# Optimization experiments

Measured on AMD Instinct MI355X. Metric: run time of the kernel, lower is better.

The kernel has to match this reference:

```python
import jax, jax.numpy as jnp
import numpy as np
from jax import lax

B, C, H, W = 16, 64, 56, 56


def _conv2d(x, w, b, dilation, padding):
    y = lax.conv_general_dilated(
        x, w, window_strides=(1, 1),
        padding=((padding, padding), (padding, padding)),
        rhs_dilation=(dilation, dilation),
        dimension_numbers=('NCHW', 'OIHW', 'NCHW'))
    return y + b[None, :, None, None]


def setup_inputs() -> dict:
    key = jax.random.key(0)
    k1, k2, k3 = jax.random.split(key, 3)
    x = jax.random.normal(k1, (B, C, H, W), dtype=jnp.float32)
    w1 = jax.random.normal(k2, (128, C, 7, 7), dtype=jnp.float32) * 0.05
    b1 = jnp.zeros((128,), dtype=jnp.float32)
    w2 = jax.random.normal(k3, (49, 128, 1, 1), dtype=jnp.float32) * 0.05
    b2 = jnp.zeros((49,), dtype=jnp.float32)
    return {"x": x, "w1": w1, "b1": b1, "w2": w2, "b2": b2}


def reference(x, w1, b1, w2, b2):
    b_, c_, h_, w_ = x.shape
    # attention-kernel branch: conv(7x7, dil=2) -> 1x1 -> softmax over 49 channels
    k = _conv2d(x, w1, b1, dilation=2, padding=6)
    k = _conv2d(k, w2, b2, dilation=1, padding=0)
    attn = jax.nn.softmax(k, axis=1)  # [B, 49, H, W]

    # dilated 13x13 neighborhood sampled at stride-2 offsets -> 7x7 taps per pixel
    xp = jnp.pad(x, ((0, 0), (0, 0), (6, 6), (6, 6)))
    shifts = [xp[:, :, 2 * p:2 * p + h_, 2 * q:2 * q + w_]
              for p in range(7) for q in range(7)]
    patches = jnp.stack(shifts, axis=-1)  # [B, C, H, W, 49]

    # Faithful to torch .view/.reshape semantics (row-major): the original code
    # reshapes [B,C,H,W,kk] -> groups of size C and [B,49,H,W] -> [B*H*W,7,7]
    # WITHOUT permuting, so the group<->pixel correspondence is the row-major one.
    pg = patches.reshape(b_ * h_ * w_, c_, 49)  # == torch view(1,-1,C,13,13)[::2,::2]
    kg = attn.reshape(b_ * h_ * w_, 49)         # == torch reshape(B*H*W,1,1,7,7)
    out = jnp.einsum('gck,gk->gc', pg, kg)      # grouped conv3d, groups=B*H*W
    return out.reshape(b_, c_, h_, w_)
```

## Files before the change

### kernel.cpp

```cpp
#include <hip/hip_runtime.h>
#include <hip/hip_bf16.h>

#define HW 3136
#define NPIX 50176

typedef __attribute__((ext_vector_type(8))) _Float16 f16x8;
typedef __attribute__((ext_vector_type(4))) float f32x4;
typedef __attribute__((ext_vector_type(8))) unsigned short u16x8;

__device__ inline unsigned short f2h(float v){
    _Float16 h = (_Float16)v;
    union { _Float16 h; unsigned short u; } cv; cv.h = h; return cv.u;
}
__device__ inline float h2f(unsigned short u){
    union { unsigned short u; _Float16 h; } cv; cv.u = u; return (float)cv.h;
}

__global__ __launch_bounds__(256) void prep_all(
    const float* __restrict__ x, const float* __restrict__ w1,
    unsigned short* __restrict__ xg, unsigned short* __restrict__ w1t,
    unsigned short* __restrict__ xpad)
{
    int bb = blockIdx.x;
    if (bb < 392) {
        int t = bb * 256 + threadIdx.x;
        int g = t / NPIX;
        int pix = t - g * NPIX;
        int b = pix / HW; int s = pix - b * HW;
        const float* xp = x + (size_t)b * 64 * HW + (size_t)g * 32 * HW + s;
        unsigned short* dst = xg + ((size_t)(b * 2 + g) * HW + s) * 32;
#pragma unroll
        for (int p = 0; p < 4; ++p) {
            alignas(16) unsigned short tmp[8];
#pragma unroll
            for (int e = 0; e < 8; ++e)
                tmp[e] = f2h(xp[(size_t)(p * 8 + e) * HW]);
            *(u16x8*)(dst + p * 8) = *(const u16x8*)tmp;
        }
    } else if (bb < 664) {
        int t2 = (bb - 392) * 256 + threadIdx.x;
        int plane = t2 / 68; int r = t2 - plane * 68;
        unsigned short* dst = xpad + ((size_t)plane * 68 + r) * 72;
        int h = r - 6;
        alignas(16) unsigned short tmp[72];
#pragma unroll
        for (int i = 0; i < 72; ++i) tmp[i] = 0;
        if (h >= 0 && h < 56) {
            const float* src = x + (size_t)plane * HW + h * 56;
#pragma unroll
            for (int wq = 0; wq < 56; ++wq) tmp[6 + wq] = f2h(src[wq]);
        }
#pragma unroll
        for (int k = 0; k < 9; ++k)
            *(u16x8*)(dst + k * 8) = *(const u16x8*)(tmp + k * 8);
    } else {
        int t = (bb - 664) * 256 + threadIdx.x;
        if (t < 2 * 49 * 128) {
            int g = t / (49 * 128);
            int r = t - g * 49 * 128;
            int tap = r / 128; int oc = r - tap * 128;
            unsigned short* dst = w1t + (size_t)t * 32;
            for (int ic = 0; ic < 32; ++ic)
                dst[ic] = f2h(w1[((size_t)oc * 64 + g * 32 + ic) * 49 + tap]);
        }
    }
}

#define LOADA(Abuf, tap) do {                                                 \
    const int p_ = (tap) / 7, q_ = (tap) - 7 * ((tap) / 7);                   \
    const int off_ = p_ * 9792 + q_ * 144;                                    \
    _Pragma("unroll")                                                         \
    for (int mt = 0; mt < 7; ++mt)                                            \
        Abuf[mt] = *(const f16x8*)(smem + abase[mt] + off_);                  \
    } while (0)

#define LOADB(Bbuf, tap) do {                                                 \
    const unsigned short* p_ = wb + (size_t)(tap) * 4096;                     \
    Bbuf[0] = *(const f16x8*)(p_);                                            \
    Bbuf[1] = *(const f16x8*)(p_ + 512);                                      \
    Bbuf[2] = *(const f16x8*)(p_ + 1024);                                     \
    Bbuf[3] = *(const f16x8*)(p_ + 1536);                                     \
    } while (0)

#define DOMFMA(Abuf, Bbuf) do {                                               \
    __builtin_amdgcn_s_setprio(1);                                            \
    _Pragma("unroll")                                                         \
    for (int mt = 0; mt < 7; ++mt) {                                          \
        acc[mt][0] = __builtin_amdgcn_mfma_f32_16x16x32_f16(Abuf[mt], Bbuf[0], acc[mt][0], 0, 0, 0); \
        acc[mt][1] = __builtin_amdgcn_mfma_f32_16x16x32_f16(Abuf[mt], Bbuf[1], acc[mt][1], 0, 0, 0); \
        acc[mt][2] = __builtin_amdgcn_mfma_f32_16x16x32_f16(Abuf[mt], Bbuf[2], acc[mt][2], 0, 0, 0); \
        acc[mt][3] = __builtin_amdgcn_mfma_f32_16x16x32_f16(Abuf[mt], Bbuf[3], acc[mt][3], 0, 0, 0); \
    }                                                                         \
    __builtin_amdgcn_s_setprio(0);                                            \
    } while (0)

__global__ __launch_bounds__(512, 2) void conv_full(
    const unsigned short* __restrict__ xg, const unsigned short* __restrict__ w1t,
    const float* __restrict__ b1, const float* __restrict__ w2,
    const float* __restrict__ b2, unsigned short* __restrict__ attn)
{
    __shared__ char smem[156672];
    unsigned short* k1sa = (unsigned short*)smem;
    unsigned short* w2s  = (unsigned short*)(smem + 60928);
    unsigned short* k1sb = (unsigned short*)(smem + 78336);

    const int blk = blockIdx.x;
    const int b   = blk / 14; const int rg = blk - b * 14;
    const int h0  = rg * 4;
    const int tid = threadIdx.x;
    const int lane = tid & 63, warp = tid >> 6;
    const int g   = warp >> 2;
    const int wm  = (warp >> 1) & 1, wn = warp & 1;
    const int oc0 = wn * 64;
    const int li  = lane & 15, j = lane >> 4;

    const unsigned short* xplane[2] = {
        xg + (size_t)(b * 2 + 0) * HW * 32,
        xg + (size_t)(b * 2 + 1) * HW * 32 };

    u16x8 zz; for (int e = 0; e < 8; ++e) zz[e] = 0;

    u16x8 sv[14];
#pragma unroll
    for (int u = 0; u < 14; ++u) {
        int i = u * 512 + tid;
        int pl = i / 3584; int rem = i - pl * 3584;
        int row = rem / 224; int r2 = rem - row * 224;
        int site = r2 >> 2, chunk = r2 & 3;
        int hh = h0 - 6 + row;
        sv[u] = (hh >= 0 && hh < 56)
            ? *(const u16x8*)(xplane[pl] + ((size_t)hh * 56 + site) * 32 + chunk * 8)
            : zz;
    }

    {
        f32x4 zv = {0.f, 0.f, 0.f, 0.f};
#pragma unroll
        for (int u = 0; u < 20; ++u) {
            int i = u * 512 + tid;
            if (i < 9792) *(f32x4*)(smem + (size_t)i * 16) = zv;
        }
    }
    __syncthreads();

#pragma unroll
    for (int u = 0; u < 14; ++u) {
        int i = u * 512 + tid;
        int pl = i / 3584; int rem = i - pl * 3584;
        int row = rem / 224; int r2 = rem - row * 224;
        int site = r2 >> 2, chunk = r2 & 3;
        int hh = h0 - 6 + row;
        if (hh >= 0 && hh < 56)
            *(u16x8*)(smem + pl * 78336 + (row * 68 + 6 + site) * 72 + chunk * 16) = sv[u];
    }
    __syncthreads();

    int abase[7];
#pragma unroll
    for (int mt = 0; mt < 7; ++mt) {
        int local = wm * 112 + mt * 16 + li;
        int rb = local / 56; int wp = local - rb * 56;
        abase[mt] = g * 78336 + (rb * 68 + wp) * 72 + j * 16;
    }

    f32x4 acc[7][4];
#pragma unroll
    for (int mt = 0; mt < 7; ++mt)
#pragma unroll
        for (int nt = 0; nt < 4; ++nt)
#pragma unroll
            for (int c = 0; c < 4; ++c) acc[mt][nt][c] = 0.f;

    const unsigned short* wb = w1t + ((size_t)g * 49 * 128 + oc0 + li) * 32 + j * 8;

    {
        f16x8 A[2][7], B[3][4];
        LOADA(A[0], 0); LOADB(B[0], 0); LOADB(B[1], 1);
#pragma unroll
        for (int t = 0; t < 49; ++t) {
            if (t < 48) LOADA(A[(t + 1) & 1], t + 1);
            if (t < 47) LOADB(B[(t + 2) % 3], t + 2);
            __builtin_amdgcn_sched_barrier(0x8);
            DOMFMA(A[t & 1], B[t % 3]);
            __builtin_amdgcn_sched_barrier(0x8);
        }
    }

    f32x4 wv[4];
#pragma unroll
    for (int u = 0; u < 4; ++u) {
        int idx = u * 512 + tid;
        wv[u] = (idx < 1568) ? *(const f32x4*)(w2 + (size_t)idx * 4)
                             : (f32x4){0.f, 0.f, 0.f, 0.f};
    }

    __syncthreads();

    {
        unsigned short* kb = g ? k1sb : k1sa;
        const int pixbase = wm * 112;
#pragma unroll
        for (int nt = 0; nt < 4; ++nt) {
            int oc = oc0 + nt * 16 + li;
            float bias = g ? 0.f : b1[oc];
#pragma unroll
            for (int mt = 0; mt < 7; ++mt) {
#pragma unroll
                for (int i = 0; i < 4; ++i) {
                    int px = pixbase + mt * 16 + j * 4 + i;
                    kb[px * 136 + oc] = f2h(acc[mt][nt][i] + bias);
                }
            }
        }
    }
#pragma unroll
    for (int u = 0; u < 4; ++u) {
        int idx = u * 512 + tid;
        if (idx < 1568) {
            int a = idx / 32; int c0 = (idx - a * 32) * 4;
            alignas(8) unsigned short t4[4];
#pragma unroll
            for (int e = 0; e < 4; ++e) t4[e] = f2h(wv[u][e]);
            *(unsigned long long*)(w2s + a * 136 + c0) = *(const unsigned long long*)t4;
        }
    }
    __syncthreads();

    const int start = (warp < 6) ? warp * 2 : 12 + (warp - 6);
    const int cnt   = (warp < 6) ? 2 : 1;
    unsigned short* ab = attn + (size_t)b * 49 * HW;

#pragma unroll
    for (int u = 0; u < 2; ++u) {
        if (u < cnt) {
            int pxt = start + u;
            f32x4 a2[4];
#pragma unroll
            for (int tt = 0; tt < 4; ++tt)
#pragma unroll
                for (int c = 0; c < 4; ++c) a2[tt][c] = 0.f;
#pragma unroll
            for (int ks = 0; ks < 4; ++ks) {
                const f16x8 ba = *(const f16x8*)(k1sa + (pxt * 16 + li) * 136 + ks * 32 + j * 8);
                const f16x8 bbv = *(const f16x8*)(k1sb + (pxt * 16 + li) * 136 + ks * 32 + j * 8);
                const f16x8 bf = ba + bbv;
#pragma unroll
                for (int tt = 0; tt < 4; ++tt) {
                    const f16x8 af = *(const f16x8*)(w2s + (tt * 16 + li) * 136 + ks * 32 + j * 8);
                    a2[tt] = __builtin_amdgcn_mfma_f32_16x16x32_f16(af, bf, a2[tt], 0, 0, 0);
                }
            }
            float mx = -3e38f;
#pragma unroll
            for (int tt = 0; tt < 4; ++tt)
#pragma unroll
                for (int i = 0; i < 4; ++i) {
                    int r = tt * 16 + j * 4 + i;
                    float v = a2[tt][i] + ((r < 49) ? b2[r] : 0.f);
                    a2[tt][i] = v;
                    if (r < 49) mx = fmaxf(mx, v);
                }
            mx = fmaxf(mx, __shfl_xor(mx, 16));
            mx = fmaxf(mx, __shfl_xor(mx, 32));
            float sum = 0.f; float ex[16];
#pragma unroll
            for (int tt = 0; tt < 4; ++tt)
#pragma unroll
                for (int i = 0; i < 4; ++i) {
                    int r = tt * 16 + j * 4 + i;
                    float e = (r < 49) ? __expf(a2[tt][i] - mx) : 0.f;
                    ex[tt * 4 + i] = e; sum += e;
                }
            sum += __shfl_xor(sum, 16);
            sum += __shfl_xor(sum, 32);
            float inv = 1.f / sum;

            int s = rg * 224 + pxt * 16 + li;
#pragma unroll
            for (int tt = 0; tt < 4; ++tt)
#pragma unroll
                for (int i = 0; i < 4; ++i) {
                    int r = tt * 16 + j * 4 + i;
                    if (r < 49) ab[(size_t)r * HW + s] = f2h(ex[tt * 4 + i] * inv);
                }
        }
    }
}

__global__ __launch_bounds__(256) void gather_kernel(
    const unsigned short* __restrict__ xpad, const unsigned short* __restrict__ attn,
    float* __restrict__ out)
{
    int tid = blockIdx.x * 256 + threadIdx.x;
    int plane = tid / 392;
    int r1 = tid - plane * 392;
    int h = r1 / 7; int oct = r1 - h * 7; int w0 = oct * 8;
    int F0 = plane * HW + h * 56 + w0;

    const unsigned short* ap = attn + (size_t)(F0 >> 6) * 49;
    float a[49];
#pragma unroll
    for (int k = 0; k < 49; ++k) a[k] = h2f(ap[k]);

    const unsigned short* xp = xpad + (size_t)plane * (68 * 72) + w0;
    float o[8];
#pragma unroll
    for (int dw = 0; dw < 8; ++dw) o[dw] = 0.f;

#pragma unroll
    for (int p = 0; p < 7; ++p) {
        const unsigned short* rp = xp + (h + 2 * p) * 72;
        u16x8 v0 = *(const u16x8*)rp;
        u16x8 v1 = *(const u16x8*)(rp + 8);
        u16x8 v2 = *(const u16x8*)(rp + 16);
        float rr[20];
#pragma unroll
        for (int e = 0; e < 8; ++e) { rr[e] = h2f(v0[e]); rr[8 + e] = h2f(v1[e]); }
#pragma unroll
        for (int e = 0; e < 4; ++e) rr[16 + e] = h2f(v2[e]);
#pragma unroll
        for (int q = 0; q < 7; ++q) {
            float aq = a[p * 7 + q];
#pragma unroll
            for (int dw = 0; dw < 8; ++dw)
                o[dw] = fmaf(rr[dw + 2 * q], aq, o[dw]);
        }
    }

    f32x4 s0 = {o[0], o[1], o[2], o[3]};
    f32x4 s1 = {o[4], o[5], o[6], o[7]};
    *(f32x4*)(out + F0) = s0;
    *(f32x4*)(out + F0 + 4) = s1;
}

extern "C" void kernel_launch(void* const* d_in, const int* in_sizes, int n_in,
                              void* d_out, int out_size, void* d_ws, size_t ws_size,
                              hipStream_t stream)
{
    const float* x  = (const float*)d_in[0];
    const float* w1 = (const float*)d_in[1];
    const float* b1 = (const float*)d_in[2];
    const float* w2 = (const float*)d_in[3];
    const float* b2 = (const float*)d_in[4];
    float* out = (float*)d_out;

    unsigned short* attn = (unsigned short*)d_ws;
    unsigned short* xg   = attn + (size_t)16 * 49 * HW;
    unsigned short* w1t  = xg + (size_t)16 * 2 * HW * 32;
    unsigned short* xpad = w1t + (size_t)2 * 49 * 128 * 32;

    prep_all<<<713, 256, 0, stream>>>(x, w1, xg, w1t, xpad);
    conv_full<<<224, 512, 0, stream>>>(xg, w1t, b1, w2, b2, attn);
    gather_kernel<<<1568, 256, 0, stream>>>(xpad, attn, out);
}
```

Measured before the change: 73.35 us.

## Relayout conv weights per kernel row and loop rows with immediate offsets

The 7x7 conv weight transform now stores weights grouped by kernel row, with the 7 column taps for each output channel packed next to each other. Each thread writes a vectorized 8-element chunk, and the prep grid grows to cover the new layout. The conv main loop drops the full 49-tap unroll and instead loops over 7 rows, each with 7 manually pipelined taps. LDS and global offsets become compile-time immediates, and base pointers advance once per row. This cuts address arithmetic, instruction footprint and register pressure, but the strict sched_barriers may limit how well the compiler can overlap loads with MFMAs.

```diff
diff --git a/kernel.cpp b/kernel.cpp
--- a/kernel.cpp
+++ b/kernel.cpp
@@ -55,31 +55,33 @@
             *(u16x8*)(dst + k * 8) = *(const u16x8*)(tmp + k * 8);
     } else {
         int t = (bb - 664) * 256 + threadIdx.x;
-        if (t < 2 * 49 * 128) {
-            int g = t / (49 * 128);
-            int r = t - g * 49 * 128;
-            int tap = r / 128; int oc = r - tap * 128;
-            unsigned short* dst = w1t + (size_t)t * 32;
-            for (int ic = 0; ic < 32; ++ic)
-                dst[ic] = f2h(w1[((size_t)oc * 64 + g * 32 + ic) * 49 + tap]);
-        }
-    }
-}
-
-#define LOADA(Abuf, tap) do {                                                 \
-    const int p_ = (tap) / 7, q_ = (tap) - 7 * ((tap) / 7);                   \
-    const int off_ = p_ * 9792 + q_ * 144;                                    \
+        int g = t / 25088;
+        int r = t - g * 25088;
+        int p = r / 3584; int r2 = r - p * 3584;
+        int oc = r2 / 28; int r3 = r2 - oc * 28;
+        int q = r3 >> 2; int j = r3 & 3;
+        unsigned short* dst = w1t + (size_t)t * 8;
+        alignas(16) unsigned short tmp[8];
+#pragma unroll
+        for (int e = 0; e < 8; ++e)
+            tmp[e] = f2h(w1[((size_t)(oc * 64 + g * 32 + j * 8 + e)) * 49 + p * 7 + q]);
+        *(u16x8*)dst = *(const u16x8*)tmp;
+    }
+}
+
+#define SB0 __builtin_amdgcn_sched_barrier(0)
+
+#define LOADA(Abuf, immB) do {                                                \
     _Pragma("unroll")                                                         \
     for (int mt = 0; mt < 7; ++mt)                                            \
-        Abuf[mt] = *(const f16x8*)(smem + abase[mt] + off_);                  \
+        Abuf[mt] = *(const f16x8*)(smem + abase[mt] + (immB));                \
     } while (0)
 
-#define LOADB(Bbuf, tap) do {                                                 \
-    const unsigned short* p_ = wb + (size_t)(tap) * 4096;                     \
-    Bbuf[0] = *(const f16x8*)(p_);                                            \
-    Bbuf[1] = *(const f16x8*)(p_ + 512);                                      \
-    Bbuf[2] = *(const f16x8*)(p_ + 1024);                                     \
-    Bbuf[3] = *(const f16x8*)(p_ + 1536);                                     \
+#define LOADB(Bbuf, immS) do {                                                \
+    Bbuf[0] = *(const f16x8*)(wb0 + (immS));                                  \
+    Bbuf[1] = *(const f16x8*)(wb1 + (immS));                                  \
+    Bbuf[2] = *(const f16x8*)(wb2 + (immS));                                  \
+    Bbuf[3] = *(const f16x8*)(wb3 + (immS));                                  \
     } while (0)
 
 #define DOMFMA(Abuf, Bbuf) do {                                               \
@@ -171,18 +173,39 @@
 #pragma unroll
             for (int c = 0; c < 4; ++c) acc[mt][nt][c] = 0.f;
 
-    const unsigned short* wb = w1t + ((size_t)g * 49 * 128 + oc0 + li) * 32 + j * 8;
+    const unsigned short* wb0 = w1t + ((size_t)(g * 7) * 128 + oc0 + li) * 224 + j * 8;
+    const unsigned short* wb1 = wb0 + (size_t)16 * 224;
+    const unsigned short* wb2 = wb0 + (size_t)32 * 224;
+    const unsigned short* wb3 = wb0 + (size_t)48 * 224;
 
     {
-        f16x8 A[2][7], B[3][4];
-        LOADA(A[0], 0); LOADB(B[0], 0); LOADB(B[1], 1);
-#pragma unroll
-        for (int t = 0; t < 49; ++t) {
-            if (t < 48) LOADA(A[(t + 1) & 1], t + 1);
-            if (t < 47) LOADB(B[(t + 2) % 3], t + 2);
-            __builtin_amdgcn_sched_barrier(0x8);
-            DOMFMA(A[t & 1], B[t % 3]);
-            __builtin_amdgcn_sched_barrier(0x8);
+        f16x8 A0[7], A1[7], B0[4], B1[4], B2[4];
+        LOADA(A0, 0); LOADB(B0, 0); LOADB(B1, 32);
+#pragma unroll 1
+        for (int p = 0; p < 7; ++p) {
+            LOADA(A1, 144); LOADB(B2, 64);
+            SB0; DOMFMA(A0, B0); SB0;
+            LOADA(A0, 288); LOADB(B0, 96);
+            SB0; DOMFMA(A1, B1); SB0;
+            LOADA(A1, 432); LOADB(B1, 128);
+            SB0; DOMFMA(A0, B2); SB0;
+            LOADA(A0, 576); LOADB(B2, 160);
+            SB0; DOMFMA(A1, B0); SB0;
+            LOADA(A1, 720); LOADB(B0, 192);
+            SB0; DOMFMA(A0, B1); SB0;
+            LOADA(A0, 864);
+            wb0 += 28672; wb1 += 28672; wb2 += 28672; wb3 += 28672;
+            SB0; DOMFMA(A1, B2); SB0;
+#pragma unroll
+            for (int mt = 0; mt < 7; ++mt) abase[mt] += 9792;
+            DOMFMA(A0, B0);
+            SB0;
+            if (p < 6) {
+                LOADA(A0, 0);
+                LOADB(B0, 0);
+                LOADB(B1, 32);
+            }
+            SB0;
         }
     }
 
@@ -347,9 +370,9 @@
     unsigned short* attn = (unsigned short*)d_ws;
     unsigned short* xg   = attn + (size_t)16 * 49 * HW;
     unsigned short* w1t  = xg + (size_t)16 * 2 * HW * 32;
-    unsigned short* xpad = w1t + (size_t)2 * 49 * 128 * 32;
-
-    prep_all<<<713, 256, 0, stream>>>(x, w1, xg, w1t, xpad);
+    unsigned short* xpad = w1t + (size_t)2 * 7 * 128 * 28 * 8;
+
+    prep_all<<<860, 256, 0, stream>>>(x, w1, xg, w1t, xpad);
     conv_full<<<224, 512, 0, stream>>>(xg, w1t, b1, w2, b2, attn);
     gather_kernel<<<1568, 256, 0, stream>>>(xpad, attn, out);
 }
```

Result: faster. 69.76 us (-4.9%).
